# Performance work log

Measured on AMD Instinct MI355X. Metric: run time of the kernel, lower is better.

## Reference

```python
import jax, jax.numpy as jnp
import numpy as np
from jax import lax

EPS = float(np.finfo(np.float64).eps)  # matches np.finfo(float).eps in torch module
C, K = 32, 128   # coarse_num, event_num
B, T, TP = 4, 512, 1024


def _fine_probs(cf_logits, ftc):
    # p(fine k | coarse c(k)) : softmax of logits restricted to each coarse group
    e = jnp.exp(cf_logits - jnp.max(cf_logits))            # [K]
    denom = jax.ops.segment_sum(e, ftc, num_segments=C)    # [C]
    return e / denom[ftc]                                  # [K]


def setup_inputs() -> dict:
    key = jax.random.key(0)
    ks = jax.random.split(key, 7)
    past_event = jax.random.randint(ks[0], (B, T), 0, C)                     # coarse ids of past events
    dt = jax.random.uniform(ks[1], (B, T), minval=0.0, maxval=0.1)
    past_time = jnp.cumsum(dt, axis=-1).astype(jnp.float32)                  # increasing event times
    horizon = float(T) * 0.05
    time_tensor = jax.random.uniform(ks[2], (B, TP), minval=0.0, maxval=horizon).astype(jnp.float32)
    mu = 0.1 * jax.random.normal(ks[3], (C,), dtype=jnp.float32)
    alpha = 0.1 * jax.random.normal(ks[4], (C, C), dtype=jnp.float32)
    delta = 0.1 * jax.random.normal(ks[5], (C, C), dtype=jnp.float32)
    cf_logits = 0.1 * jax.random.normal(ks[6], (K,), dtype=jnp.float32)
    ftc = jnp.arange(K) % C                                                   # fine -> coarse map
    return dict(past_event=past_event, past_time=past_time, time_tensor=time_tensor,
                mu=mu, alpha=alpha, delta=delta, cf_logits=cf_logits, ftc=ftc)


def reference(past_event, past_time, time_tensor, mu, alpha, delta, cf_logits, ftc):
    Bb, Tp = time_tensor.shape
    Cc = mu.shape[0]
    past_alpha = jax.nn.softplus(alpha)[past_event]          # [B,T,C]
    past_delta = jax.nn.softplus(delta)[past_event] + EPS    # [B,T,C]

    def step(acc, xs):
        pa_i, pd_i, pt_i = xs                                # [B,C],[B,C],[B]
        et = time_tensor - pt_i[:, None]                     # [B,Tp]
        use = (et > EPS).astype(acc.dtype)                   # causal mask
        etc = jnp.where(et < EPS, 0.0, et)
        effect = pa_i[:, None, :] * jnp.exp(-pd_i[:, None, :] * etc[:, :, None])  # [B,Tp,C]
        return acc + effect * use[:, :, None], None

    acc0 = jnp.zeros((Bb, Tp, Cc), dtype=time_tensor.dtype)
    acc, _ = lax.scan(step, acc0,
                      (past_alpha.transpose(1, 0, 2), past_delta.transpose(1, 0, 2), past_time.T))
    all_inten = acc + jax.nn.softplus(mu)[None, None, :]     # [B,Tp,C]
    fine_inten = all_inten[..., ftc] * _fine_probs(cf_logits, ftc)  # [B,Tp,K]
    return fine_inten
```

## Files before the change

### kernel.cpp

```cpp
#include <hip/hip_runtime.h>

#define BB   4
#define TT   512
#define TPN  1024
#define CC   32
#define KK   128
#define EPSF 2.220446049250313e-16f
#define LOG2E 1.4426950408889634f

#if __has_builtin(__builtin_amdgcn_exp2f)
#define EXP2F(x) __builtin_amdgcn_exp2f(x)
#else
#define EXP2F(x) exp2f(x)
#endif

__device__ __forceinline__ float softplus_f(float x) {
    return fmaxf(x, 0.f) + log1pf(__expf(-fabsf(x)));
}

__global__ __launch_bounds__(256) void GHP_prep(
    const float* __restrict__ mu, const float* __restrict__ alpha,
    const float* __restrict__ delta, const float* __restrict__ cf_logits,
    const int* __restrict__ ftc, float2* __restrict__ ws2)
{
    const int tid = threadIdx.x;
    for (int idx = tid; idx < CC * CC; idx += 256) {
        float a = softplus_f(alpha[idx]);
        float d = (softplus_f(delta[idx]) + EPSF) * LOG2E;
        ws2[idx] = make_float2(a, d);
    }
    if (tid < KK) {
        float mx = -1e30f;
        for (int j = 0; j < KK; ++j) mx = fmaxf(mx, cf_logits[j]);
        const int myc = ftc[tid];
        const float e = __expf(cf_logits[tid] - mx);
        float den = 0.f;
        for (int j = 0; j < KK; ++j) {
            float ej = __expf(cf_logits[j] - mx);
            den += (ftc[j] == myc) ? ej : 0.f;
        }
        const float p = e / den;
        ws2[CC * CC + tid] = make_float2(p, softplus_f(mu[myc]) * p);
    }
}

__global__ __launch_bounds__(256, 8) void GHP_main(
    const int*   __restrict__ past_event,
    const float* __restrict__ past_time,
    const float* __restrict__ time_tensor,
    const int*   __restrict__ ftc,
    const float2* __restrict__ ws2,
    float*       __restrict__ out)
{
    __shared__ __align__(16) float2 sad_s[CC * CC];
    __shared__ __align__(16) float2 ptev_s[4 * 128];
    __shared__ __align__(16) float2 pk_s[KK];
    __shared__ int   ftc_s[KK];
    __shared__ float part_s[2 * 4 * CC];

    const int tid = threadIdx.x;
    const int b   = blockIdx.x >> 9;
    const int tp0 = (blockIdx.x & 511) << 1;

    {
        const float4* src = (const float4*)ws2;
        float4* dst = (float4*)sad_s;
        dst[tid]       = src[tid];
        dst[tid + 256] = src[tid + 256];
    }
    if (tid < 64) ((float4*)pk_s)[tid] = ((const float4*)(ws2 + CC * CC))[tid];
    if (tid < KK) ftc_s[tid] = ftc[tid];
    for (int i = tid; i < TT; i += 256) {
        const int r = i & 3, j = i >> 2;
        ptev_s[(r << 7) + j] = make_float2(past_time[b * TT + i],
                                           __int_as_float(past_event[b * TT + i] << 5));
    }
    __syncthreads();

    const int c   = tid & 31;
    const int h   = (tid >> 5) & 1;
    const int w   = (tid >> 6) & 1;
    const int tpl = tid >> 7;
    const int r   = (w << 1) + h;
    const float t = time_tensor[b * TPN + tp0 + tpl];

    const float2* pp = ptev_s + (r << 7);
    int lo = 0, hi = 128;
    #pragma unroll
    for (int s = 0; s < 8; ++s) {
        const int mid = (lo + hi) >> 1;
        const bool go = (lo < hi) && ((t - pp[mid].x) > EPSF);
        lo = go ? mid + 1 : lo;
        hi = go ? hi : mid;
    }
    const int J = lo;

    float acc0 = 0.f, acc1 = 0.f;
    int j = 0;
    #pragma unroll 2
    for (; j + 4 <= J; j += 4) {
        const float4 q0 = *(const float4*)(pp + j);
        const float4 q1 = *(const float4*)(pp + j + 2);
        const float2 ad0 = sad_s[__float_as_int(q0.y) + c];
        const float2 ad1 = sad_s[__float_as_int(q0.w) + c];
        const float2 ad2 = sad_s[__float_as_int(q1.y) + c];
        const float2 ad3 = sad_s[__float_as_int(q1.w) + c];
        acc0 = fmaf(ad0.x, EXP2F(-ad0.y * (t - q0.x)), acc0);
        acc1 = fmaf(ad1.x, EXP2F(-ad1.y * (t - q0.z)), acc1);
        acc0 = fmaf(ad2.x, EXP2F(-ad2.y * (t - q1.x)), acc0);
        acc1 = fmaf(ad3.x, EXP2F(-ad3.y * (t - q1.z)), acc1);
    }
    for (; j < J; ++j) {
        const float2 pe = pp[j];
        const float2 ad = sad_s[__float_as_int(pe.y) + c];
        acc0 = fmaf(ad.x, EXP2F(-ad.y * (t - pe.x)), acc0);
    }
    part_s[((tpl << 2) + r) * CC + c] = acc0 + acc1;
    __syncthreads();

    {
        const int k   = tid & 127;
        const int tpe = tid >> 7;
        const int ck  = ftc_s[k];
        const float* ps = part_s + (tpe << 7);
        const float inten = (ps[ck] + ps[CC + ck]) + (ps[2 * CC + ck] + ps[3 * CC + ck]);
        const float2 pv = pk_s[k];
        out[(size_t)(b * TPN + tp0 + tpe) * KK + k] = fmaf(inten, pv.x, pv.y);
    }
}

extern "C" void kernel_launch(void* const* d_in, const int* in_sizes, int n_in,
                              void* d_out, int out_size, void* d_ws, size_t ws_size,
                              hipStream_t stream) {
    const int*   past_event  = (const int*)  d_in[0];
    const float* past_time   = (const float*)d_in[1];
    const float* time_tensor = (const float*)d_in[2];
    const float* mu          = (const float*)d_in[3];
    const float* alpha       = (const float*)d_in[4];
    const float* delta       = (const float*)d_in[5];
    const float* cf_logits   = (const float*)d_in[6];
    const int*   ftc         = (const int*)  d_in[7];
    float*       out         = (float*)d_out;
    float2*      ws2         = (float2*)d_ws;

    GHP_prep<<<1, 256, 0, stream>>>(mu, alpha, delta, cf_logits, ftc, ws2);
    GHP_main<<<BB * (TPN / 2), 256, 0, stream>>>(past_event, past_time, time_tensor,
                                                 ftc, ws2, out);
}
```

Measured before the change: 91.93 us.

## Fuse parameter prep kernel into main kernel, recomputing softplus per block

Removes the single-block prep kernel and its launch and global workspace round-trip by having every block compute the softplus tables, mu softplus and per-group softmax denominators into shared memory. The denominator uses shared atomics after the barrier and drops max-subtraction, relying on small logits to avoid overflow. The trade is redundant transcendental work in each of 2048 blocks, in exchange for one fewer launch and no serial dependency between kernels.

```diff
diff --git a/kernel.cpp b/kernel.cpp
--- a/kernel.cpp
+++ b/kernel.cpp
@@ -18,64 +18,51 @@
     return fmaxf(x, 0.f) + log1pf(__expf(-fabsf(x)));
 }
 
-__global__ __launch_bounds__(256) void GHP_prep(
-    const float* __restrict__ mu, const float* __restrict__ alpha,
-    const float* __restrict__ delta, const float* __restrict__ cf_logits,
-    const int* __restrict__ ftc, float2* __restrict__ ws2)
-{
-    const int tid = threadIdx.x;
-    for (int idx = tid; idx < CC * CC; idx += 256) {
-        float a = softplus_f(alpha[idx]);
-        float d = (softplus_f(delta[idx]) + EPSF) * LOG2E;
-        ws2[idx] = make_float2(a, d);
-    }
-    if (tid < KK) {
-        float mx = -1e30f;
-        for (int j = 0; j < KK; ++j) mx = fmaxf(mx, cf_logits[j]);
-        const int myc = ftc[tid];
-        const float e = __expf(cf_logits[tid] - mx);
-        float den = 0.f;
-        for (int j = 0; j < KK; ++j) {
-            float ej = __expf(cf_logits[j] - mx);
-            den += (ftc[j] == myc) ? ej : 0.f;
-        }
-        const float p = e / den;
-        ws2[CC * CC + tid] = make_float2(p, softplus_f(mu[myc]) * p);
-    }
-}
-
-__global__ __launch_bounds__(256, 8) void GHP_main(
+__global__ __launch_bounds__(256, 8) void GHP_fused(
     const int*   __restrict__ past_event,
     const float* __restrict__ past_time,
     const float* __restrict__ time_tensor,
+    const float* __restrict__ mu,
+    const float* __restrict__ alpha,
+    const float* __restrict__ delta,
+    const float* __restrict__ cf_logits,
     const int*   __restrict__ ftc,
-    const float2* __restrict__ ws2,
     float*       __restrict__ out)
 {
     __shared__ __align__(16) float2 sad_s[CC * CC];
     __shared__ __align__(16) float2 ptev_s[4 * 128];
-    __shared__ __align__(16) float2 pk_s[KK];
+    __shared__ float e_s[KK];
     __shared__ int   ftc_s[KK];
+    __shared__ float den_s[CC];
+    __shared__ float spmu_s[CC];
     __shared__ float part_s[2 * 4 * CC];
 
     const int tid = threadIdx.x;
     const int b   = blockIdx.x >> 9;
     const int tp0 = (blockIdx.x & 511) << 1;
 
-    {
-        const float4* src = (const float4*)ws2;
-        float4* dst = (float4*)sad_s;
-        dst[tid]       = src[tid];
-        dst[tid + 256] = src[tid + 256];
+    #pragma unroll
+    for (int idx = tid; idx < CC * CC; idx += 256) {
+        const float a = softplus_f(alpha[idx]);
+        const float d = (softplus_f(delta[idx]) + EPSF) * LOG2E;
+        sad_s[idx] = make_float2(a, d);
     }
-    if (tid < 64) ((float4*)pk_s)[tid] = ((const float4*)(ws2 + CC * CC))[tid];
-    if (tid < KK) ftc_s[tid] = ftc[tid];
+    #pragma unroll
     for (int i = tid; i < TT; i += 256) {
         const int r = i & 3, j = i >> 2;
         ptev_s[(r << 7) + j] = make_float2(past_time[b * TT + i],
                                            __int_as_float(past_event[b * TT + i] << 5));
     }
+    if (tid < KK) {
+        e_s[tid] = __expf(cf_logits[tid]);
+        ftc_s[tid] = ftc[tid];
+    }
+    if (tid < CC) {
+        den_s[tid]  = 0.f;
+        spmu_s[tid] = softplus_f(mu[tid]);
+    }
     __syncthreads();
+    if (tid < KK) atomicAdd(&den_s[ftc_s[tid]], e_s[tid]);
 
     const int c   = tid & 31;
     const int h   = (tid >> 5) & 1;
@@ -123,9 +110,10 @@
         const int tpe = tid >> 7;
         const int ck  = ftc_s[k];
         const float* ps = part_s + (tpe << 7);
-        const float inten = (ps[ck] + ps[CC + ck]) + (ps[2 * CC + ck] + ps[3 * CC + ck]);
-        const float2 pv = pk_s[k];
-        out[(size_t)(b * TPN + tp0 + tpe) * KK + k] = fmaf(inten, pv.x, pv.y);
+        const float inten = ((ps[ck] + ps[CC + ck]) + (ps[2 * CC + ck] + ps[3 * CC + ck]))
+                            + spmu_s[ck];
+        const float p = e_s[k] / den_s[ck];
+        out[(size_t)(b * TPN + tp0 + tpe) * KK + k] = inten * p;
     }
 }
 
@@ -141,9 +129,7 @@
     const float* cf_logits   = (const float*)d_in[6];
     const int*   ftc         = (const int*)  d_in[7];
     float*       out         = (float*)d_out;
-    float2*      ws2         = (float2*)d_ws;
 
-    GHP_prep<<<1, 256, 0, stream>>>(mu, alpha, delta, cf_logits, ftc, ws2);
-    GHP_main<<<BB * (TPN / 2), 256, 0, stream>>>(past_event, past_time, time_tensor,
-                                                 ftc, ws2, out);
+    GHP_fused<<<BB * (TPN / 2), 256, 0, stream>>>(past_event, past_time, time_tensor,
+                                                  mu, alpha, delta, cf_logits, ftc, out);
 }
```

After: 87.32 us. 5.0% less time.
